# Optimization experiments

Hardware: AMD Instinct MI355X
Metric: run time of the kernel (lower is better)

The kernel has to match this reference:

```python
import jax, jax.numpy as jnp
import numpy as np

B, S, DIM = 2, 2048, 2048
NH, NKV, HD = 32, 8, 64
N_REP = NH // NKV


def apply_rope(x, cos, sin):
    # x: (B, H, S, HD); cos/sin: (S, HD//2)
    d = x.shape[-1] // 2
    x1, x2 = x[..., :d], x[..., d:]
    c = cos[None, None, :, :]
    s = sin[None, None, :, :]
    return jnp.concatenate([x1 * c - x2 * s, x2 * c + x1 * s], axis=-1)


def setup_inputs() -> dict:
    key = jax.random.key(0)
    ks = jax.random.split(key, 8)
    x = jax.random.normal(ks[0], (B, S, DIM), dtype=jnp.float32)
    # plausible RoPE tables
    inv_freq = 1.0 / (10000.0 ** (jnp.arange(0, HD, 2, dtype=jnp.float32) / HD))
    t = jnp.arange(S, dtype=jnp.float32)
    freqs = jnp.outer(t, inv_freq)  # (S, HD//2)
    rope_cos = jnp.cos(freqs)
    rope_sin = jnp.sin(freqs)
    doc_ids = jnp.sort(jax.random.randint(ks[1], (B, S), 0, 8, dtype=jnp.int32), axis=-1)
    std = 0.02
    Wq = jax.random.normal(ks[2], (NH * HD, DIM), dtype=jnp.float32) * std
    Wk = jax.random.normal(ks[3], (NKV * HD, DIM), dtype=jnp.float32) * std
    Wv = jax.random.normal(ks[4], (NKV * HD, DIM), dtype=jnp.float32) * std
    Wo = jax.random.normal(ks[5], (DIM, NH * HD), dtype=jnp.float32) * std
    return {"x": x, "rope_cos": rope_cos, "rope_sin": rope_sin,
            "doc_ids": doc_ids, "Wq": Wq, "Wk": Wk, "Wv": Wv, "Wo": Wo}


def reference(x, rope_cos, rope_sin, doc_ids, Wq, Wk, Wv, Wo):
    batch, seq_len, _ = x.shape
    q = (x @ Wq.T).reshape(batch, seq_len, NH, HD).transpose(0, 2, 1, 3)   # (B,NH,S,HD)
    k = (x @ Wk.T).reshape(batch, seq_len, NKV, HD).transpose(0, 2, 1, 3)  # (B,NKV,S,HD)
    v = (x @ Wv.T).reshape(batch, seq_len, NKV, HD).transpose(0, 2, 1, 3)

    q = apply_rope(q, rope_cos, rope_sin)
    k = apply_rope(k, rope_cos, rope_sin)

    # GQA expansion (repeat_interleave on head dim)
    k = jnp.repeat(k, N_REP, axis=1)  # (B,NH,S,HD)
    v = jnp.repeat(v, N_REP, axis=1)

    # block-diagonal causal mask from packed doc ids
    doc_mask = doc_ids[:, :, None] == doc_ids[:, None, :]          # (B,S,S)
    causal = jnp.tril(jnp.ones((seq_len, seq_len), dtype=bool))    # (S,S)
    mask = (doc_mask & causal[None])[:, None, :, :]                # (B,1,S,S)

    scale = 1.0 / jnp.sqrt(jnp.asarray(HD, dtype=q.dtype))
    scores = jnp.einsum("bhqd,bhkd->bhqk", q, k) * scale
    scores = jnp.where(mask, scores, jnp.finfo(scores.dtype).min)
    attn = jax.nn.softmax(scores, axis=-1)
    out = jnp.einsum("bhqk,bhkd->bhqd", attn, v)                   # (B,NH,S,HD)
    out = out.transpose(0, 2, 1, 3).reshape(batch, seq_len, NH * HD)
    return out @ Wo.T
```

## Files before the change

### kernel.cpp

```cpp
#include <hip/hip_runtime.h>
#include <hip/hip_bf16.h>

#define BB   2
#define SEQ  2048
#define DIMD 2048
#define NHH  32
#define NKVV 8
#define HDD  64
#define QKVS 3072

typedef __bf16 bf16x8 __attribute__((ext_vector_type(8)));
typedef float  floatx4 __attribute__((ext_vector_type(4)));

typedef __attribute__((address_space(1))) const void* gas_ptr;
typedef __attribute__((address_space(3))) void*       las_ptr;

#define MFMA16 __builtin_amdgcn_mfma_f32_16x16x32_bf16
#define CBAR() asm volatile("" ::: "memory")
#define EXP2F(x) __builtin_amdgcn_exp2f(x)

__device__ __forceinline__ unsigned short f2bu(float f) {
    __hip_bfloat16 h = __float2bfloat16(f);
    return *reinterpret_cast<unsigned short*>(&h);
}

#define DPPF(x, ctrl) __int_as_float(__builtin_amdgcn_mov_dpp(__float_as_int(x), (ctrl), 0xF, 0xF, true))
__device__ __forceinline__ float red16_max(float x) {
    x = fmaxf(x, DPPF(x, 0xB1));
    x = fmaxf(x, DPPF(x, 0x4E));
    x = fmaxf(x, DPPF(x, 0x124));
    x = fmaxf(x, DPPF(x, 0x128));
    return x;
}
__device__ __forceinline__ float red16_sum(float x) {
    x += DPPF(x, 0xB1);
    x += DPPF(x, 0x4E);
    x += DPPF(x, 0x124);
    x += DPPF(x, 0x128);
    return x;
}

#define C_X  (8u  * 1024 * 1024)
#define C_WQ (4u  * 1024 * 1024)
#define C_WK (1u  * 1024 * 1024)
#define C_WV (1u  * 1024 * 1024)
#define C_WO (4u  * 1024 * 1024)
__global__ void cvt_all(const float* __restrict__ x,  const float* __restrict__ wq,
                        const float* __restrict__ wk, const float* __restrict__ wv,
                        const float* __restrict__ wo,
                        __hip_bfloat16* __restrict__ xb,
                        __hip_bfloat16* __restrict__ wqkv,
                        __hip_bfloat16* __restrict__ wob)
{
    unsigned i = (blockIdx.x * blockDim.x + threadIdx.x) * 4;
    const float* src; __hip_bfloat16* dst;
    if (i < C_X)                       { src = x  + i;                    dst = xb + i; }
    else if (i < C_X + C_WQ)           { unsigned o = i - C_X;            src = wq + o; dst = wqkv + o; }
    else if (i < C_X + C_WQ + C_WK)    { unsigned o = i - C_X - C_WQ;     src = wk + o; dst = wqkv + C_WQ + o; }
    else if (i < C_X + C_WQ + C_WK + C_WV) { unsigned o = i - C_X - C_WQ - C_WK; src = wv + o; dst = wqkv + C_WQ + C_WK + o; }
    else                               { unsigned o = i - C_X - C_WQ - C_WK - C_WV; if (o >= C_WO) return; src = wo + o; dst = wob + o; }
    float4 v = *reinterpret_cast<const float4*>(src);
    dst[0] = __float2bfloat16(v.x);
    dst[1] = __float2bfloat16(v.y);
    dst[2] = __float2bfloat16(v.z);
    dst[3] = __float2bfloat16(v.w);
}

template <typename OutT, bool ROPE>
__global__ __launch_bounds__(256) void gemm_lds(
    const __hip_bfloat16* __restrict__ Abf,
    const __hip_bfloat16* __restrict__ Wbf,
    OutT* __restrict__ C,
    int M, int N, int K, int ldc,
    const float* __restrict__ cosb, const float* __restrict__ sinb,
    unsigned short* __restrict__ vT)
{
    const __bf16* A = reinterpret_cast<const __bf16*>(Abf);
    const __bf16* W = reinterpret_cast<const __bf16*>(Wbf);

    __shared__ __bf16 As[128 * 32];
    __shared__ __bf16 Bs[128 * 32];

    int tid  = threadIdx.x;
    int wid  = tid >> 6;
    int lane = tid & 63;
    int l15  = lane & 15;
    int l4   = lane >> 4;
    int wm   = (wid & 1) * 64;
    int wn   = (wid >> 1) * 64;
    int bm   = blockIdx.x * 128;
    int bn   = blockIdx.y * 128;

    int r0 = tid >> 2,         g0 = (tid & 3) ^ ((r0 >> 1) & 3);
    int r1 = (tid + 256) >> 2, g1 = (tid & 3) ^ ((r1 >> 1) & 3);

    const __bf16* a0 = A + (size_t)(bm + r0) * K + g0 * 8;
    const __bf16* a1 = A + (size_t)(bm + r1) * K + g1 * 8;
    const __bf16* w0 = W + (size_t)(bn + r0) * K + g0 * 8;
    const __bf16* w1 = W + (size_t)(bn + r1) * K + g1 * 8;

    __bf16* lA0 = As + tid * 8;
    __bf16* lA1 = As + (tid + 256) * 8;
    __bf16* lB0 = Bs + tid * 8;
    __bf16* lB1 = Bs + (tid + 256) * 8;

    int arow[4], aslot[4], brow[4], bslot[4];
    #pragma unroll
    for (int i = 0; i < 4; ++i) {
        int ra = wm + i * 16 + l15;
        int rb = wn + i * 16 + l15;
        arow[i] = ra; aslot[i] = l4 ^ ((ra >> 1) & 3);
        brow[i] = rb; bslot[i] = l4 ^ ((rb >> 1) & 3);
    }

    floatx4 acc[4][4] = {};

    for (int k0 = 0; k0 < K; k0 += 32) {
        __builtin_amdgcn_global_load_lds((gas_ptr)(a0 + k0), (las_ptr)lA0, 16, 0, 0);
        __builtin_amdgcn_global_load_lds((gas_ptr)(a1 + k0), (las_ptr)lA1, 16, 0, 0);
        __builtin_amdgcn_global_load_lds((gas_ptr)(w0 + k0), (las_ptr)lB0, 16, 0, 0);
        __builtin_amdgcn_global_load_lds((gas_ptr)(w1 + k0), (las_ptr)lB1, 16, 0, 0);
        __syncthreads();

        bf16x8 af[4], bfr[4];
        #pragma unroll
        for (int i = 0; i < 4; ++i)
            af[i] = *reinterpret_cast<const bf16x8*>(As + arow[i] * 32 + aslot[i] * 8);
        #pragma unroll
        for (int j = 0; j < 4; ++j)
            bfr[j] = *reinterpret_cast<const bf16x8*>(Bs + brow[j] * 32 + bslot[j] * 8);

        #pragma unroll
        for (int i = 0; i < 4; ++i)
            #pragma unroll
            for (int j = 0; j < 4; ++j)
                acc[i][j] = MFMA16(af[i], bfr[j], acc[i][j], 0, 0, 0);
        __syncthreads();
    }

    const int col0 = bn + wn;
    if constexpr (ROPE) {
        if (col0 >= 2560) {
            int kvh = (col0 - 2560) >> 6;
            int b   = bm >> 11;
            int s0  = (bm & (SEQ - 1)) + wm + l4 * 4;
            #pragma unroll
            for (int i = 0; i < 4; ++i)
                #pragma unroll
                for (int ni = 0; ni < 4; ++ni) {
                    int d = ni * 16 + l15;
                    ushort4 u;
                    u.x = f2bu(acc[i][ni][0]);
                    u.y = f2bu(acc[i][ni][1]);
                    u.z = f2bu(acc[i][ni][2]);
                    u.w = f2bu(acc[i][ni][3]);
                    *reinterpret_cast<ushort4*>(
                        vT + ((size_t)(b * NKVV + kvh) * 64 + d) * SEQ + s0 + i * 16) = u;
                }
        } else {
            #pragma unroll
            for (int i = 0; i < 4; ++i) {
                #pragma unroll
                for (int r = 0; r < 4; ++r) {
                    int row = bm + wm + i * 16 + l4 * 4 + r;
                    int s   = row & (SEQ - 1);
                    #pragma unroll
                    for (int j = 0; j < 2; ++j) {
                        float x1 = acc[i][j][r], x2 = acc[i][j + 2][r];
                        float cf = cosb[s * 32 + j * 16 + l15];
                        float sf = sinb[s * 32 + j * 16 + l15];
                        float o1 = x1 * cf - x2 * sf;
                        float o2 = x2 * cf + x1 * sf;
                        int col = col0 + j * 16 + l15;
                        C[(size_t)row * ldc + col]      = __float2bfloat16(o1);
                        C[(size_t)row * ldc + col + 32] = __float2bfloat16(o2);
                    }
                }
            }
        }
    } else {
        #pragma unroll
        for (int i = 0; i < 4; ++i)
            #pragma unroll
            for (int j = 0; j < 4; ++j)
                #pragma unroll
                for (int r = 0; r < 4; ++r) {
                    int row = bm + wm + i * 16 + l4 * 4 + r;
                    int col = col0 + j * 16 + l15;
                    if constexpr (sizeof(OutT) == 4)
                        C[(size_t)row * ldc + col] = acc[i][j][r];
                    else
                        C[(size_t)row * ldc + col] = __float2bfloat16(acc[i][j][r]);
                }
    }
}

#define SCL2 0.18033688f
#define MASKV -3e30f

__global__ __launch_bounds__(256) void attn_mfma(
    const __hip_bfloat16* __restrict__ qkv,
    const unsigned short* __restrict__ vT,
    const int* __restrict__ doc,
    __hip_bfloat16* __restrict__ ob)
{
    int qblk = (int)gridDim.x - 1 - (int)blockIdx.x;
    int h    = blockIdx.y;
    int b    = blockIdx.z;
    int kvh  = h >> 2;
    int tid  = threadIdx.x;
    int wv   = tid >> 6;
    int lane = tid & 63;
    int l15  = lane & 15;
    int l4   = lane >> 4;
    int q0   = qblk * 128;
    int qw   = q0 + wv * 32;

    __shared__ unsigned short Ks[2][64 * 64];
    __shared__ unsigned short Vts[2][64 * 64];
    __shared__ int            kdoc[2][64];
    __shared__ unsigned short Pb[4][32][76];

    const unsigned short* qus = reinterpret_cast<const unsigned short*>(qkv);
    const unsigned short* kus = qus + 2048;
    const int* docb = doc + b * SEQ;

    bf16x8 aq[2][2];
    #pragma unroll
    for (int qt = 0; qt < 2; ++qt) {
        const unsigned short* qrow = qus + (size_t)(b * SEQ + qw + qt * 16 + l15) * QKVS + h * HDD;
        aq[qt][0] = *reinterpret_cast<const bf16x8*>(qrow + l4 * 8);
        aq[qt][1] = *reinterpret_cast<const bf16x8*>(qrow + 32 + l4 * 8);
    }
    int qd[2][4];
    #pragma unroll
    for (int qt = 0; qt < 2; ++qt)
        #pragma unroll
        for (int r = 0; r < 4; ++r)
            qd[qt][r] = docb[qw + qt * 16 + l4 * 4 + r];
    int qd_w   = docb[qw];
    int qd_w31 = docb[qw + 31];
    int qd_blk = docb[q0];
    bool qdu   = (qd_w == qd_w31);

    float mrow[2][4], lrow[2][4];
    #pragma unroll
    for (int qt = 0; qt < 2; ++qt)
        #pragma unroll
        for (int r = 0; r < 4; ++r) { mrow[qt][r] = -1e30f; lrow[qt][r] = 0.f; }
    floatx4 accO[2][4] = {};

    int slot0 = tid, slot1 = tid + 256;
    int row0 = slot0 >> 3, g0 = (slot0 & 7) ^ (row0 & 7);
    int row1 = slot1 >> 3, g1 = (slot1 & 7) ^ (row1 & 7);
    const unsigned short* vtb = vT + ((size_t)(b * NKVV + kvh) * 64) * SEQ;

    int kc_end = 2 * qblk + 1;
    unsigned mask;
    {
        bool v = false;
        if (lane <= kc_end && lane < 32)
            v = (docb[lane * 64 + 63] >= qd_blk);
        mask = (unsigned)__ballot(v);
    }

    auto stagec = [&](int buf, int kc) {
        int k0 = kc * 64;
        __builtin_amdgcn_global_load_lds(
            (gas_ptr)(kus + (size_t)(b * SEQ + k0 + row0) * QKVS + kvh * HDD + g0 * 8),
            (las_ptr)(&Ks[buf][slot0 * 8]), 16, 0, 0);
        __builtin_amdgcn_global_load_lds(
            (gas_ptr)(kus + (size_t)(b * SEQ + k0 + row1) * QKVS + kvh * HDD + g1 * 8),
            (las_ptr)(&Ks[buf][slot1 * 8]), 16, 0, 0);
        __builtin_amdgcn_global_load_lds(
            (gas_ptr)(vtb + (size_t)row0 * SEQ + k0 + g0 * 8),
            (las_ptr)(&Vts[buf][slot0 * 8]), 16, 0, 0);
        __builtin_amdgcn_global_load_lds(
            (gas_ptr)(vtb + (size_t)row1 * SEQ + k0 + g1 * 8),
            (las_ptr)(&Vts[buf][slot1 * 8]), 16, 0, 0);
        __builtin_amdgcn_global_load_lds(
            (gas_ptr)(docb + k0 + lane),
            (las_ptr)(&kdoc[buf][lane]), 4, 0, 0);
    };

    int p  = 0;
    int kc = (int)__builtin_ctz(mask);
    mask &= mask - 1;
    stagec(0, kc);

    while (true) {
        int nkc = -1;
        if (mask) {
            nkc = (int)__builtin_ctz(mask);
            mask &= mask - 1;
            stagec(p ^ 1, nkc);
            asm volatile("s_waitcnt vmcnt(5)" ::: "memory");
        } else {
            asm volatile("s_waitcnt vmcnt(0)" ::: "memory");
        }
        CBAR(); __builtin_amdgcn_s_barrier(); CBAR();

        int k0 = kc * 64;
        int kd_first = kdoc[p][0];
        int kd_last  = kdoc[p][63];
        if (k0 <= qw + 31 && kd_last >= qd_w) {
            bool full = qdu && (kd_first == kd_last) && (kd_last == qd_w)
                        && (k0 + 64 <= qw);

            bf16x8 bk[4][2];
            #pragma unroll
            for (int t = 0; t < 4; ++t) {
                int krow = t * 16 + l15;
                bk[t][0] = *reinterpret_cast<const bf16x8*>(&Ks[p][krow * 64 + ((l4 ^ (krow & 7)) * 8)]);
                bk[t][1] = *reinterpret_cast<const bf16x8*>(&Ks[p][krow * 64 + (((l4 + 4) ^ (krow & 7)) * 8)]);
            }

            #pragma unroll
            for (int qt = 0; qt < 2; ++qt) {
                float s[4][4];
                #pragma unroll
                for (int t = 0; t < 4; ++t) {
                    floatx4 a = {};
                    a = MFMA16(aq[qt][0], bk[t][0], a, 0, 0, 0);
                    a = MFMA16(aq[qt][1], bk[t][1], a, 0, 0, 0);
                    if (full) {
                        #pragma unroll
                        for (int r = 0; r < 4; ++r) s[t][r] = a[r] * SCL2;
                    } else {
                        int key = k0 + t * 16 + l15;
                        int kd  = kdoc[p][t * 16 + l15];
                        #pragma unroll
                        for (int r = 0; r < 4; ++r) {
                            int qrow = qw + qt * 16 + l4 * 4 + r;
                            bool valid = (kd == qd[qt][r]) && (key <= qrow);
                            s[t][r] = valid ? a[r] * SCL2 : MASKV;
                        }
                    }
                }
                #pragma unroll
                for (int r = 0; r < 4; ++r) {
                    float pm = fmaxf(fmaxf(s[0][r], s[1][r]), fmaxf(s[2][r], s[3][r]));
                    pm = red16_max(pm);
                    float mnew = fmaxf(mrow[qt][r], pm);
                    float alpha = EXP2F(mrow[qt][r] - mnew);
                    mrow[qt][r] = mnew;
                    float ps = 0.f;
                    #pragma unroll
                    for (int t = 0; t < 4; ++t) {
                        float pv = EXP2F(s[t][r] - mnew);
                        Pb[wv][qt * 16 + l4 * 4 + r][t * 16 + l15] = f2bu(pv);
                        ps += pv;
                    }
                    ps = red16_sum(ps);
                    lrow[qt][r] = lrow[qt][r] * alpha + ps;
                    #pragma unroll
                    for (int t = 0; t < 4; ++t) accO[qt][t][r] *= alpha;
                }
            }

            bf16x8 bvf[4][2];
            #pragma unroll
            for (int t = 0; t < 4; ++t) {
                int vrow = t * 16 + l15;
                bvf[t][0] = *reinterpret_cast<const bf16x8*>(&Vts[p][vrow * 64 + ((l4 ^ (vrow & 7)) * 8)]);
                bvf[t][1] = *reinterpret_cast<const bf16x8*>(&Vts[p][vrow * 64 + (((l4 + 4) ^ (vrow & 7)) * 8)]);
            }
            #pragma unroll
            for (int qt = 0; qt < 2; ++qt) {
                bf16x8 ap0 = *reinterpret_cast<const bf16x8*>(&Pb[wv][qt * 16 + l15][l4 * 8]);
                bf16x8 ap1 = *reinterpret_cast<const bf16x8*>(&Pb[wv][qt * 16 + l15][32 + l4 * 8]);
                #pragma unroll
                for (int t = 0; t < 4; ++t) {
                    accO[qt][t] = MFMA16(ap0, bvf[t][0], accO[qt][t], 0, 0, 0);
                    accO[qt][t] = MFMA16(ap1, bvf[t][1], accO[qt][t], 0, 0, 0);
                }
            }
        }
        CBAR(); __builtin_amdgcn_s_barrier(); CBAR();
        if (nkc < 0) break;
        kc = nkc; p ^= 1;
    }

    #pragma unroll
    for (int qt = 0; qt < 2; ++qt)
        #pragma unroll
        for (int r = 0; r < 4; ++r) {
            float inv = 1.0f / lrow[qt][r];
            size_t base = (size_t)(b * SEQ + qw + qt * 16 + l4 * 4 + r) * (NHH * HDD) + h * HDD;
            #pragma unroll
            for (int t = 0; t < 4; ++t)
                ob[base + t * 16 + l15] = __float2bfloat16(accO[qt][t][r] * inv);
        }
}

extern "C" void kernel_launch(void* const* d_in, const int* in_sizes, int n_in,
                              void* d_out, int out_size, void* d_ws, size_t ws_size,
                              hipStream_t stream) {
    const float* x  = (const float*)d_in[0];
    const float* rc = (const float*)d_in[1];
    const float* rs = (const float*)d_in[2];
    const int*   dc = (const int*)d_in[3];
    const float* Wq = (const float*)d_in[4];
    const float* Wk = (const float*)d_in[5];
    const float* Wv = (const float*)d_in[6];
    const float* Wo = (const float*)d_in[7];
    float* out = (float*)d_out;

    const int M    = BB * SEQ;
    const int KVD  = NKVV * HDD;
    const int QKVN = DIMD + 2 * KVD;

    char* ws = (char*)d_ws;
    size_t off = 0;
    auto alloc = [&](size_t elems) { __hip_bfloat16* p = (__hip_bfloat16*)(ws + off); off += elems * 2; return p; };
    __hip_bfloat16* xb   = alloc((size_t)M * DIMD);
    __hip_bfloat16* wqkv = alloc((size_t)QKVN * DIMD);
    __hip_bfloat16* wob  = alloc((size_t)DIMD * DIMD);
    __hip_bfloat16* qkv  = alloc((size_t)M * QKVN);
    __hip_bfloat16* abuf = alloc((size_t)M * DIMD);
    unsigned short* vtb  = (unsigned short*)alloc((size_t)BB * NKVV * HDD * SEQ);

    {
        unsigned total4 = (C_X + C_WQ + C_WK + C_WV + C_WO) / 4;
        cvt_all<<<dim3((total4 + 255) / 256), 256, 0, stream>>>(
            x, Wq, Wk, Wv, Wo, xb, wqkv, wob);
    }

    gemm_lds<__hip_bfloat16, true><<<dim3(M / 128, QKVN / 128), 256, 0, stream>>>(
        xb, wqkv, qkv, M, QKVN, DIMD, QKVN, rc, rs, vtb);

    attn_mfma<<<dim3(SEQ / 128, NHH, BB), 256, 0, stream>>>(qkv, vtb, dc, abuf);

    gemm_lds<float, false><<<dim3(M / 128, DIMD / 128), 256, 0, stream>>>(
        abuf, wob, out, M, DIMD, DIMD, DIMD, nullptr, nullptr, nullptr);
}
```

Measured before the change: 276.4 us.

## Switch GEMMs to 32x32x16 MFMA with a 64-wide K tile

Both projection GEMMs now use 32x32x16 bf16 MFMA in place of 16x16x32 MFMA, and the K step per LDS stage grows from 32 to 64. The LDS swizzle becomes an XOR over 8 chunks. The RoPE, V-transpose and plain output epilogues are rewritten for the 32x32 accumulator layout. The aim is to halve the number of sync pairs per K and cut LDS fragment reads per MFMA, at the cost of twice the LDS per block and still no double buffering.

```diff
diff --git a/kernel.cpp b/kernel.cpp
--- a/kernel.cpp
+++ b/kernel.cpp
@@ -10,12 +10,14 @@
 #define QKVS 3072
 
 typedef __bf16 bf16x8 __attribute__((ext_vector_type(8)));
-typedef float  floatx4 __attribute__((ext_vector_type(4)));
+typedef float  floatx4  __attribute__((ext_vector_type(4)));
+typedef float  floatx16 __attribute__((ext_vector_type(16)));
 
 typedef __attribute__((address_space(1))) const void* gas_ptr;
 typedef __attribute__((address_space(3))) void*       las_ptr;
 
 #define MFMA16 __builtin_amdgcn_mfma_f32_16x16x32_bf16
+#define MFMA32 __builtin_amdgcn_mfma_f32_32x32x16_bf16
 #define CBAR() asm volatile("" ::: "memory")
 #define EXP2F(x) __builtin_amdgcn_exp2f(x)
 
@@ -67,7 +69,7 @@
 }
 
 template <typename OutT, bool ROPE>
-__global__ __launch_bounds__(256) void gemm_lds(
+__global__ __launch_bounds__(256) void gemm32(
     const __hip_bfloat16* __restrict__ Abf,
     const __hip_bfloat16* __restrict__ Wbf,
     OutT* __restrict__ C,
@@ -78,63 +80,63 @@
     const __bf16* A = reinterpret_cast<const __bf16*>(Abf);
     const __bf16* W = reinterpret_cast<const __bf16*>(Wbf);
 
-    __shared__ __bf16 As[128 * 32];
-    __shared__ __bf16 Bs[128 * 32];
+    __shared__ __bf16 As[128 * 64];
+    __shared__ __bf16 Bs[128 * 64];
 
     int tid  = threadIdx.x;
     int wid  = tid >> 6;
     int lane = tid & 63;
-    int l15  = lane & 15;
-    int l4   = lane >> 4;
+    int l31  = lane & 31;
+    int lh   = lane >> 5;
     int wm   = (wid & 1) * 64;
     int wn   = (wid >> 1) * 64;
     int bm   = blockIdx.x * 128;
     int bn   = blockIdx.y * 128;
 
-    int r0 = tid >> 2,         g0 = (tid & 3) ^ ((r0 >> 1) & 3);
-    int r1 = (tid + 256) >> 2, g1 = (tid & 3) ^ ((r1 >> 1) & 3);
-
-    const __bf16* a0 = A + (size_t)(bm + r0) * K + g0 * 8;
-    const __bf16* a1 = A + (size_t)(bm + r1) * K + g1 * 8;
-    const __bf16* w0 = W + (size_t)(bn + r0) * K + g0 * 8;
-    const __bf16* w1 = W + (size_t)(bn + r1) * K + g1 * 8;
-
-    __bf16* lA0 = As + tid * 8;
-    __bf16* lA1 = As + (tid + 256) * 8;
-    __bf16* lB0 = Bs + tid * 8;
-    __bf16* lB1 = Bs + (tid + 256) * 8;
-
-    int arow[4], aslot[4], brow[4], bslot[4];
+    const __bf16* aS[4]; const __bf16* wS[4];
     #pragma unroll
     for (int i = 0; i < 4; ++i) {
-        int ra = wm + i * 16 + l15;
-        int rb = wn + i * 16 + l15;
-        arow[i] = ra; aslot[i] = l4 ^ ((ra >> 1) & 3);
-        brow[i] = rb; bslot[i] = l4 ^ ((rb >> 1) & 3);
-    }
-
-    floatx4 acc[4][4] = {};
-
-    for (int k0 = 0; k0 < K; k0 += 32) {
-        __builtin_amdgcn_global_load_lds((gas_ptr)(a0 + k0), (las_ptr)lA0, 16, 0, 0);
-        __builtin_amdgcn_global_load_lds((gas_ptr)(a1 + k0), (las_ptr)lA1, 16, 0, 0);
-        __builtin_amdgcn_global_load_lds((gas_ptr)(w0 + k0), (las_ptr)lB0, 16, 0, 0);
-        __builtin_amdgcn_global_load_lds((gas_ptr)(w1 + k0), (las_ptr)lB1, 16, 0, 0);
+        int slot = tid + 256 * i;
+        int r = slot >> 3;
+        int c = (slot & 7) ^ (r & 7);
+        aS[i] = A + (size_t)(bm + r) * K + c * 8;
+        wS[i] = W + (size_t)(bn + r) * K + c * 8;
+    }
+
+    floatx16 acc[2][2] = {};
+
+    for (int k0 = 0; k0 < K; k0 += 64) {
+        #pragma unroll
+        for (int i = 0; i < 4; ++i)
+            __builtin_amdgcn_global_load_lds((gas_ptr)(aS[i] + k0),
+                (las_ptr)(As + (tid + 256 * i) * 8), 16, 0, 0);
+        #pragma unroll
+        for (int i = 0; i < 4; ++i)
+            __builtin_amdgcn_global_load_lds((gas_ptr)(wS[i] + k0),
+                (las_ptr)(Bs + (tid + 256 * i) * 8), 16, 0, 0);
         __syncthreads();
 
-        bf16x8 af[4], bfr[4];
-        #pragma unroll
-        for (int i = 0; i < 4; ++i)
-            af[i] = *reinterpret_cast<const bf16x8*>(As + arow[i] * 32 + aslot[i] * 8);
-        #pragma unroll
-        for (int j = 0; j < 4; ++j)
-            bfr[j] = *reinterpret_cast<const bf16x8*>(Bs + brow[j] * 32 + bslot[j] * 8);
-
-        #pragma unroll
-        for (int i = 0; i < 4; ++i)
-            #pragma unroll
-            for (int j = 0; j < 4; ++j)
-                acc[i][j] = MFMA16(af[i], bfr[j], acc[i][j], 0, 0, 0);
+        #pragma unroll
+        for (int s = 0; s < 4; ++s) {
+            bf16x8 af[2], bfr[2];
+            #pragma unroll
+            for (int mt = 0; mt < 2; ++mt) {
+                int row = wm + mt * 32 + l31;
+                int ch  = (s * 2 + lh) ^ (row & 7);
+                af[mt] = *reinterpret_cast<const bf16x8*>(As + row * 64 + ch * 8);
+            }
+            #pragma unroll
+            for (int nt = 0; nt < 2; ++nt) {
+                int row = wn + nt * 32 + l31;
+                int ch  = (s * 2 + lh) ^ (row & 7);
+                bfr[nt] = *reinterpret_cast<const bf16x8*>(Bs + row * 64 + ch * 8);
+            }
+            #pragma unroll
+            for (int mt = 0; mt < 2; ++mt)
+                #pragma unroll
+                for (int nt = 0; nt < 2; ++nt)
+                    acc[mt][nt] = MFMA32(af[mt], bfr[nt], acc[mt][nt], 0, 0, 0);
+        }
         __syncthreads();
     }
 
@@ -143,54 +145,52 @@
         if (col0 >= 2560) {
             int kvh = (col0 - 2560) >> 6;
             int b   = bm >> 11;
-            int s0  = (bm & (SEQ - 1)) + wm + l4 * 4;
-            #pragma unroll
-            for (int i = 0; i < 4; ++i)
-                #pragma unroll
-                for (int ni = 0; ni < 4; ++ni) {
-                    int d = ni * 16 + l15;
-                    ushort4 u;
-                    u.x = f2bu(acc[i][ni][0]);
-                    u.y = f2bu(acc[i][ni][1]);
-                    u.z = f2bu(acc[i][ni][2]);
-                    u.w = f2bu(acc[i][ni][3]);
-                    *reinterpret_cast<ushort4*>(
-                        vT + ((size_t)(b * NKVV + kvh) * 64 + d) * SEQ + s0 + i * 16) = u;
+            #pragma unroll
+            for (int mt = 0; mt < 2; ++mt)
+                #pragma unroll
+                for (int rq = 0; rq < 4; ++rq) {
+                    int s0 = (bm & (SEQ - 1)) + wm + mt * 32 + rq * 8 + lh * 4;
+                    #pragma unroll
+                    for (int nt = 0; nt < 2; ++nt) {
+                        int d = nt * 32 + l31;
+                        ushort4 u;
+                        u.x = f2bu(acc[mt][nt][rq * 4 + 0]);
+                        u.y = f2bu(acc[mt][nt][rq * 4 + 1]);
+                        u.z = f2bu(acc[mt][nt][rq * 4 + 2]);
+                        u.w = f2bu(acc[mt][nt][rq * 4 + 3]);
+                        *reinterpret_cast<ushort4*>(
+                            vT + ((size_t)(b * NKVV + kvh) * 64 + d) * SEQ + s0) = u;
+                    }
                 }
         } else {
             #pragma unroll
-            for (int i = 0; i < 4; ++i) {
-                #pragma unroll
-                for (int r = 0; r < 4; ++r) {
-                    int row = bm + wm + i * 16 + l4 * 4 + r;
+            for (int mt = 0; mt < 2; ++mt)
+                #pragma unroll
+                for (int reg = 0; reg < 16; ++reg) {
+                    int row = bm + wm + mt * 32 + (reg & 3) + (reg >> 2) * 8 + lh * 4;
                     int s   = row & (SEQ - 1);
-                    #pragma unroll
-                    for (int j = 0; j < 2; ++j) {
-                        float x1 = acc[i][j][r], x2 = acc[i][j + 2][r];
-                        float cf = cosb[s * 32 + j * 16 + l15];
-                        float sf = sinb[s * 32 + j * 16 + l15];
-                        float o1 = x1 * cf - x2 * sf;
-                        float o2 = x2 * cf + x1 * sf;
-                        int col = col0 + j * 16 + l15;
-                        C[(size_t)row * ldc + col]      = __float2bfloat16(o1);
-                        C[(size_t)row * ldc + col + 32] = __float2bfloat16(o2);
-                    }
-                }
-            }
+                    float x1 = acc[mt][0][reg], x2 = acc[mt][1][reg];
+                    float cf = cosb[s * 32 + l31];
+                    float sf = sinb[s * 32 + l31];
+                    float o1 = x1 * cf - x2 * sf;
+                    float o2 = x2 * cf + x1 * sf;
+                    C[(size_t)row * ldc + col0 + l31]      = __float2bfloat16(o1);
+                    C[(size_t)row * ldc + col0 + 32 + l31] = __float2bfloat16(o2);
+                }
         }
     } else {
         #pragma unroll
-        for (int i = 0; i < 4; ++i)
-            #pragma unroll
-            for (int j = 0; j < 4; ++j)
-                #pragma unroll
-                for (int r = 0; r < 4; ++r) {
-                    int row = bm + wm + i * 16 + l4 * 4 + r;
-                    int col = col0 + j * 16 + l15;
+        for (int mt = 0; mt < 2; ++mt)
+            #pragma unroll
+            for (int nt = 0; nt < 2; ++nt)
+                #pragma unroll
+                for (int reg = 0; reg < 16; ++reg) {
+                    int row = bm + wm + mt * 32 + (reg & 3) + (reg >> 2) * 8 + lh * 4;
+                    int col = col0 + nt * 32 + l31;
                     if constexpr (sizeof(OutT) == 4)
-                        C[(size_t)row * ldc + col] = acc[i][j][r];
+                        C[(size_t)row * ldc + col] = acc[mt][nt][reg];
                     else
-                        C[(size_t)row * ldc + col] = __float2bfloat16(acc[i][j][r]);
+                        C[(size_t)row * ldc + col] = __float2bfloat16(acc[mt][nt][reg]);
                 }
     }
 }
@@ -426,11 +426,11 @@
             x, Wq, Wk, Wv, Wo, xb, wqkv, wob);
     }
 
-    gemm_lds<__hip_bfloat16, true><<<dim3(M / 128, QKVN / 128), 256, 0, stream>>>(
+    gemm32<__hip_bfloat16, true><<<dim3(M / 128, QKVN / 128), 256, 0, stream>>>(
         xb, wqkv, qkv, M, QKVN, DIMD, QKVN, rc, rs, vtb);
 
     attn_mfma<<<dim3(SEQ / 128, NHH, BB), 256, 0, stream>>>(qkv, vtb, dc, abuf);
 
-    gemm_lds<float, false><<<dim3(M / 128, DIMD / 128), 256, 0, stream>>>(
+    gemm32<float, false><<<dim3(M / 128, DIMD / 128), 256, 0, stream>>>(
         abuf, wob, out, M, DIMD, DIMD, DIMD, nullptr, nullptr, nullptr);
 }
```

Result: faster. 257.7 us (median of 2 runs) (-6.8%).
